# Performance work log

Measured on AMD Instinct MI355X. Metric: run time of the kernel, lower is better.

Reference implementation:

```python
import jax, jax.numpy as jnp
import numpy as np

BORDER = 3
SHIFTS = 2 * BORDER + 1  # 7 shifts per axis -> 49 total


def setup_inputs() -> dict:
    key = jax.random.key(0)
    k1, k2, k3 = jax.random.split(key, 3)
    B, C, H = 64, 1, 384
    sr = jax.random.normal(k1, (B, C, H, H), dtype=jnp.float32)
    hr = jax.random.normal(k2, (B, C, H, H), dtype=jnp.float32)
    hr_mask = (jax.random.uniform(k3, (B, C, H, H)) > 0.1).astype(jnp.float32)
    return {"sr": sr, "hr": hr, "hr_mask": hr_mask}


def _cmse_masked(sr, hr, hr_mask):
    B, C, H, _ = hr.shape
    crop = H - 2 * BORDER  # size_cropped_image
    # mask sr and hr as in the torch code (done once, outside the shift loop)
    sr_m = sr * hr_mask
    pred = sr_m[:, :, BORDER:H - BORDER, BORDER:H - BORDER]  # [B,C,crop,crop]
    hr_m = hr * hr_mask

    # all 49 (i,j) shift offsets
    ij = jnp.stack(
        jnp.meshgrid(jnp.arange(SHIFTS), jnp.arange(SHIFTS), indexing="ij"), axis=-1
    ).reshape(-1, 2)  # [49, 2]

    def per_shift(carry, off):
        i, j = off[0], off[1]
        L = jax.lax.dynamic_slice(hr_m, (0, 0, i, j), (B, C, crop, crop))
        m = jax.lax.dynamic_slice(hr_mask, (0, 0, i, j), (B, C, crop, crop))
        n = jnp.sum(m, axis=(1, 2, 3))  # total_pixels_masked per sample
        b = jnp.sum(L - pred, axis=(1, 2, 3)) / n  # brightness bias correction
        corrected = (pred + b[:, None, None, None]) * m
        mse = jnp.sum(jnp.square(L - corrected), axis=(1, 2, 3)) / n  # [B]
        return carry, mse

    _, mses = jax.lax.scan(per_shift, None, ij)  # [49, B]
    min_cmse = jnp.min(mses, axis=0)  # best shift per sample
    return jnp.mean(min_cmse)


def reference(sr, hr, hr_mask):
    return _cmse_masked(sr, hr, hr_mask)
```

## Files before the change

kernel.cpp:

```cpp
#include <hip/hip_runtime.h>

#define IMG   384
#define IMG4  96
#define IMG2  (IMG*IMG)
#define CROP  378
#define NB    64
#define NGRP  16
#define NROWS 24
#define NSTR  6
#define NTH   256
#define PSTR  520

typedef __fp16 half8  __attribute__((ext_vector_type(8)));
typedef __fp16 f16x2  __attribute__((ext_vector_type(2)));
typedef float  floatx4 __attribute__((ext_vector_type(4)));

__device__ __forceinline__ unsigned pkh(float a, float b) {
    f16x2 h = __builtin_amdgcn_cvt_pkrtz(a, b);
    return __builtin_bit_cast(unsigned, h);
}

__global__ __launch_bounds__(NTH)
void corr_kernel(const float* __restrict__ sr, const float* __restrict__ hr,
                 const float* __restrict__ mk, float* __restrict__ part)
{
    __shared__ __align__(16) char qpl [16*784];
    __shared__ __align__(16) char mpl [16*784];
    __shared__ __align__(16) char ppool[2*8*800 + 16];
    __shared__ float rowQ2[32];
    char* const ppl  = ppool;
    char* const p2pl = ppool + 8*800 + 16;

    const int tid = threadIdx.x;
    const int id  = blockIdx.x;
    const int c8  = id & 7;
    const int k0  = id >> 3;
    const int b   = c8 + 8 * (k0 >> 4);
    const int grp = k0 & 15;
    const int c0  = grp * NROWS;
    const int nvalid = (CROP - c0 < NROWS) ? (CROP - c0) : NROWS;

    const float*  sb   = sr + (size_t)b * IMG2;
    const float*  mown = mk + (size_t)b * IMG2;
    const float4* hb4  = (const float4*)(hr + (size_t)b * IMG2);
    const float4* mb4  = (const float4*)(mk + (size_t)b * IMG2);

    const int wid  = tid >> 6;
    const int lane = tid & 63;
    const int m16  = lane & 15;
    const int g    = lane >> 4;

    floatx4 D0 = {0.f, 0.f, 0.f, 0.f};
    floatx4 D1 = {0.f, 0.f, 0.f, 0.f};

    const uint4 onesbits = {0x3C003C00u, 0x3C003C00u, 0x3C003C00u, 0x3C003C00u};
    const uint4 zerobits = {0u, 0u, 0u, 0u};
    const half8 ones8 = __builtin_bit_cast(half8, onesbits);
    const half8 zero8 = __builtin_bit_cast(half8, zerobits);

    float eacc = 0.f;
    int ei = 0, et = 0, ek = 0, ecolByte = 0;
    if (tid < 252) {
        ei = tid / 36; const int rem = tid % 36; et = rem % 12; ek = rem / 12;
        const int ec = (et < 6) ? et : (372 + et);
        ecolByte = 2 * ec;
    }

    float4 hvr[2], mvr[2];
    auto qm_issue = [&](int relBase) {
        #pragma unroll
        for (int k = 0; k < 2; ++k) {
            const int idx = (tid + k * 256) % 384;
            const int rw = idx / 96, c = idx % 96;
            int w = c0 + relBase + rw; if (w > 383) w = 383;
            hvr[k] = hb4[(size_t)w * IMG4 + c];
            mvr[k] = mb4[(size_t)w * IMG4 + c];
        }
    };
    auto qm_write = [&](int relBase) {
        #pragma unroll
        for (int k = 0; k < 2; ++k) {
            const int idx = (tid + k * 256) % 384;
            const int rw = idx / 96, c = idx % 96;
            const int rel = relBase + rw;
            const float4 hv = hvr[k], mv = mvr[k];
            const float qx = hv.x*mv.x, qy = hv.y*mv.y;
            const float qz = hv.z*mv.z, qw = hv.w*mv.w;
            const int slot = rel & 15;
            *(uint2*)(qpl + slot*784 + c*8) = make_uint2(pkh(qx, qy), pkh(qz, qw));
            *(uint2*)(mpl + slot*784 + c*8) = make_uint2(pkh(mv.x, mv.y), pkh(mv.z, mv.w));
            if (k == 0 || tid < 128)
                atomicAdd(&rowQ2[rel & 31], qx*qx + qy*qy + qz*qz + qw*qw);
        }
    };
    float ps0[3], ps1[3], pm0[3], pm1[3];
    auto p_issue = [&](int relBase) {
        #pragma unroll
        for (int k = 0; k < 3; ++k) {
            const int idx = (tid + k * 256) % 756;
            const int rw = idx / 189, d = 4 + idx % 189;
            int rc = relBase + rw; if (c0 + rc > 377) rc = 377 - c0;
            const int v0 = 2*d - 8;
            const float* srow = sb   + (size_t)(c0 + rc + 3) * IMG + (v0 + 3);
            const float* mrow = mown + (size_t)(c0 + rc + 3) * IMG + (v0 + 3);
            ps0[k] = srow[0]; ps1[k] = srow[1];
            pm0[k] = mrow[0]; pm1[k] = mrow[1];
        }
    };
    auto p_write = [&](int relBase) {
        #pragma unroll
        for (int k = 0; k < 3; ++k) {
            const int idx = (tid + k * 256) % 756;
            const int rw = idx / 189, d = 4 + idx % 189;
            const int rrel = relBase + rw;
            const float p0 = ps0[k] * pm0[k], p1 = ps1[k] * pm1[k];
            const int slot = rrel & 7;
            *(unsigned*)(ppl  + slot*800 + 4*d) = pkh(p0, p1);
            *(unsigned*)(p2pl + slot*800 + 4*d) = pkh(p0*p0, p1*p1);
        }
    };

    for (int idx = tid; idx < 8*2*11; idx += NTH) {
        const int slot = idx / 22, rem = idx % 22;
        const int pl = rem / 11, kk = rem % 11;
        const int dd = (kk < 4) ? kk : (189 + kk);
        *(unsigned*)((pl ? p2pl : ppl) + slot*800 + 4*dd) = 0u;
    }
    if (tid < 32) rowQ2[tid] = 0.f;
    __syncthreads();
    for (int idx = tid; idx < 10*96; idx += NTH) {
        const int rw = idx / 96, c = idx % 96;
        int w = c0 + rw; if (w > 383) w = 383;
        const float4 hv = hb4[(size_t)w * IMG4 + c];
        const float4 mv = mb4[(size_t)w * IMG4 + c];
        const float qx = hv.x*mv.x, qy = hv.y*mv.y;
        const float qz = hv.z*mv.z, qw = hv.w*mv.w;
        *(uint2*)(qpl + rw*784 + c*8) = make_uint2(pkh(qx, qy), pkh(qz, qw));
        *(uint2*)(mpl + rw*784 + c*8) = make_uint2(pkh(mv.x, mv.y), pkh(mv.z, mv.w));
        atomicAdd(&rowQ2[rw], qx*qx + qy*qy + qz*qz + qw*qw);
    }
    p_issue(0);
    p_write(0);
    __syncthreads();

    for (int s = 0; s < NSTR; ++s) {
        const bool doStage = (s < NSTR - 1);
        if (doStage) {
            qm_issue(4*s + 10);
            p_issue(4*s + 4);
        }
        __builtin_amdgcn_sched_barrier(0);

        const int lr = 4*s + wid;
        if (lr < nvalid) {
            const int mm    = (m16 < 7) ? m16 : (m16 - 7);
            const int slotA = (lr + mm) & 15;
            const char* aB = ((m16 < 7) ? qpl : mpl) + slotA*784;
            const char* bB = ((m16 < 7) ? ppl : p2pl) + (lr & 7)*800;
            const int Sb = 16 - 2*mm + g*16;
            #pragma unroll
            for (int sl = 0; sl < 12; ++sl) {
                half8 av, bv;
                if (m16 < 14) {
                    av = *(const half8*)(aB + sl*64 + g*16);
                    const int S  = Sb + sl*64;
                    const int S0 = S & ~3;
                    const unsigned sh = (unsigned)((S & 2) << 3);
                    const unsigned* bw = (const unsigned*)(bB + S0);
                    const unsigned d0 = bw[0], d1 = bw[1], d2 = bw[2], d3 = bw[3], d4 = bw[4];
                    uint4 bi;
                    bi.x = __builtin_amdgcn_alignbit(d1, d0, sh);
                    bi.y = __builtin_amdgcn_alignbit(d2, d1, sh);
                    bi.z = __builtin_amdgcn_alignbit(d3, d2, sh);
                    bi.w = __builtin_amdgcn_alignbit(d4, d3, sh);
                    bv = __builtin_bit_cast(half8, bi);
                } else if (m16 == 14) {
                    av = ones8; bv = ones8;
                } else {
                    av = zero8; bv = zero8;
                }
                if (sl & 1) D1 = __builtin_amdgcn_mfma_f32_16x16x32_f16(av, bv, D1, 0, 0, 0);
                else        D0 = __builtin_amdgcn_mfma_f32_16x16x32_f16(av, bv, D0, 0, 0, 0);
            }
        }

        if (tid < 252) {
            #pragma unroll
            for (int rr = 0; rr < 4; ++rr) {
                if (4*s + rr < nvalid) {
                    const int slot = (4*s + rr + ei) & 15;
                    const char* pl = (ek == 0) ? mpl : qpl;
                    const float v = (float)*(const __fp16*)(pl + slot*784 + ecolByte);
                    eacc += (ek == 2) ? v*v : v;
                }
            }
        }

        if (doStage) {
            qm_write(4*s + 10);
            p_write(4*s + 4);
        }
        __syncthreads();
    }

    float* wred = (float*)ppool;
    {
        const floatx4 D = D0 + D1;
        const int rb = (lane >> 4) * 4, col = lane & 15;
        #pragma unroll
        for (int k = 0; k < 4; ++k)
            wred[wid*256 + (rb + k)*16 + col] = D[k];
    }
    __syncthreads();
    float* po = part + (size_t)(b * NGRP + grp) * PSTR;
    po[tid] = wred[tid] + wred[256 + tid] + wred[512 + tid] + wred[768 + tid];
    if (tid < 7) {
        float t = 0.f;
        for (int k = 0; k < nvalid; ++k) t += rowQ2[tid + k];
        po[256 + tid] = t;
    }
    if (tid < 252)
        po[264 + ek*84 + ei*12 + et] = eacc;
}

__global__ __launch_bounds__(NTH)
void mse_kernel(const float* __restrict__ part, double* __restrict__ bmin)
{
    __shared__ double chunk[4][49][7];
    const int b   = blockIdx.x;
    const int tid = threadIdx.x;
    const int s   = tid & 63;
    const int cc  = tid >> 6;

    if (s < 49) {
        const int i = s / 7, j = s % 7;
        double A=0, Bc=0, Cc=0, Tm=0, Tq=0, Tq2=0, Sp=0;
        for (int gg = cc*4; gg < cc*4 + 4; ++gg) {
            const float* p = part + (size_t)(b * NGRP + gg) * PSTR;
            A   += p[i*16 + j];
            Cc  += p[(7+i)*16 + j];
            Bc  += p[(7+i)*16 + 7 + j];
            Tq  += p[i*16 + 14];
            Tm  += p[(7+i)*16 + 14];
            Sp  += p[14*16 + 0];
            Tq2 += p[256 + i];
            #pragma unroll
            for (int t = 0; t < 12; ++t) {
                if (t < j || t >= j + 6) {
                    Tm  -= p[264 +      i*12 + t];
                    Tq  -= p[264 + 84 + i*12 + t];
                    Tq2 -= p[264 +168 + i*12 + t];
                }
            }
        }
        chunk[cc][s][0] = A;  chunk[cc][s][1] = Bc; chunk[cc][s][2] = Cc;
        chunk[cc][s][3] = Tm; chunk[cc][s][4] = Tq; chunk[cc][s][5] = Tq2;
        chunk[cc][s][6] = Sp;
    }
    __syncthreads();

    if (tid < 64) {
        double mse = 1e300;
        if (tid < 49) {
            double v[7];
            #pragma unroll
            for (int q = 0; q < 7; ++q)
                v[q] = chunk[0][tid][q] + chunk[1][tid][q] + chunk[2][tid][q] + chunk[3][tid][q];
            const double A = v[0], Bc = v[1], Cc = v[2], Tm = v[3];
            const double Tq = v[4], Tq2 = v[5], Sp = v[6];
            const double bb = (Tq - Sp) / Tm;
            mse = (Tq2 - 2.0*A - 2.0*bb*Tq + Bc + 2.0*bb*Cc + bb*bb*Tm) / Tm;
        }
        for (int off = 32; off; off >>= 1) {
            const double o = __shfl_down(mse, off);
            mse = fmin(mse, o);
        }
        if (tid == 0) bmin[b] = mse;
    }
}

__global__ __launch_bounds__(64)
void mean_kernel(const double* __restrict__ bmin, float* __restrict__ out)
{
    double v = bmin[threadIdx.x];
    for (int off = 32; off; off >>= 1) v += __shfl_down(v, off);
    if (threadIdx.x == 0) out[0] = (float)(v / 64.0);
}

extern "C" void kernel_launch(void* const* d_in, const int* in_sizes, int n_in,
                              void* d_out, int out_size, void* d_ws, size_t ws_size,
                              hipStream_t stream) {
    const float* sr = (const float*)d_in[0];
    const float* hr = (const float*)d_in[1];
    const float* mk = (const float*)d_in[2];

    float* part = (float*)d_ws;
    const size_t part_bytes = (size_t)NB * NGRP * PSTR * sizeof(float);
    double* bmin = (double*)((char*)d_ws + part_bytes);

    corr_kernel<<<dim3(NB * NGRP), NTH, 0, stream>>>(sr, hr, mk, part);
    mse_kernel<<<dim3(NB), NTH, 0, stream>>>(part, bmin);
    mean_kernel<<<dim3(1), 64, 0, stream>>>(bmin, (float*)d_out);
}
```

Baseline: 58.63 us.

## Replace pipelined row streaming with 512-thread three-tile load-then-compute loop

```diff
diff --git a/kernel.cpp b/kernel.cpp
--- a/kernel.cpp
+++ b/kernel.cpp
@@ -7,8 +7,9 @@
 #define NB    64
 #define NGRP  16
 #define NROWS 24
-#define NSTR  6
-#define NTH   256
+#define TILES 3
+#define TROWS 8
+#define NTH   512
 #define PSTR  520
 
 typedef __fp16 half8  __attribute__((ext_vector_type(8)));
@@ -24,10 +25,10 @@
 void corr_kernel(const float* __restrict__ sr, const float* __restrict__ hr,
                  const float* __restrict__ mk, float* __restrict__ part)
 {
-    __shared__ __align__(16) char qpl [16*784];
-    __shared__ __align__(16) char mpl [16*784];
+    __shared__ __align__(16) char qpl [15*784];
+    __shared__ __align__(16) char mpl [15*784];
     __shared__ __align__(16) char ppool[2*8*800 + 16];
-    __shared__ float rowQ2[32];
+    __shared__ float rowQ2[TILES][16];
     char* const ppl  = ppool;
     char* const p2pl = ppool + 8*800 + 16;
 
@@ -66,97 +67,45 @@
         ecolByte = 2 * ec;
     }
 
-    float4 hvr[2], mvr[2];
-    auto qm_issue = [&](int relBase) {
-        #pragma unroll
-        for (int k = 0; k < 2; ++k) {
-            const int idx = (tid + k * 256) % 384;
+    if (tid < TILES*16) ((float*)rowQ2)[tid] = 0.f;
+    if (tid < 8*2*11) {
+        const int slot = tid / 22, rem = tid % 22;
+        const int pl = rem / 11, kk = rem % 11;
+        const int dd = (kk < 4) ? kk : (189 + kk);
+        *(unsigned*)((pl ? p2pl : ppl) + slot*800 + 4*dd) = 0u;
+    }
+    __syncthreads();
+
+    for (int t = 0; t < TILES; ++t) {
+        const int r0 = TROWS * t;
+
+        for (int idx = tid; idx < 15*96; idx += NTH) {
             const int rw = idx / 96, c = idx % 96;
-            int w = c0 + relBase + rw; if (w > 383) w = 383;
-            hvr[k] = hb4[(size_t)w * IMG4 + c];
-            mvr[k] = mb4[(size_t)w * IMG4 + c];
-        }
-    };
-    auto qm_write = [&](int relBase) {
-        #pragma unroll
-        for (int k = 0; k < 2; ++k) {
-            const int idx = (tid + k * 256) % 384;
-            const int rw = idx / 96, c = idx % 96;
-            const int rel = relBase + rw;
-            const float4 hv = hvr[k], mv = mvr[k];
+            int w = c0 + r0 + rw; if (w > 383) w = 383;
+            const float4 hv = hb4[(size_t)w * IMG4 + c];
+            const float4 mv = mb4[(size_t)w * IMG4 + c];
             const float qx = hv.x*mv.x, qy = hv.y*mv.y;
             const float qz = hv.z*mv.z, qw = hv.w*mv.w;
-            const int slot = rel & 15;
-            *(uint2*)(qpl + slot*784 + c*8) = make_uint2(pkh(qx, qy), pkh(qz, qw));
-            *(uint2*)(mpl + slot*784 + c*8) = make_uint2(pkh(mv.x, mv.y), pkh(mv.z, mv.w));
-            if (k == 0 || tid < 128)
-                atomicAdd(&rowQ2[rel & 31], qx*qx + qy*qy + qz*qz + qw*qw);
-        }
-    };
-    float ps0[3], ps1[3], pm0[3], pm1[3];
-    auto p_issue = [&](int relBase) {
-        #pragma unroll
-        for (int k = 0; k < 3; ++k) {
-            const int idx = (tid + k * 256) % 756;
+            *(uint2*)(qpl + rw*784 + c*8) = make_uint2(pkh(qx, qy), pkh(qz, qw));
+            *(uint2*)(mpl + rw*784 + c*8) = make_uint2(pkh(mv.x, mv.y), pkh(mv.z, mv.w));
+            atomicAdd(&rowQ2[t][rw], qx*qx + qy*qy + qz*qz + qw*qw);
+        }
+        for (int idx = tid; idx < 8*189; idx += NTH) {
             const int rw = idx / 189, d = 4 + idx % 189;
-            int rc = relBase + rw; if (c0 + rc > 377) rc = 377 - c0;
+            int rc = r0 + rw; if (c0 + rc > 377) rc = 377 - c0;
             const int v0 = 2*d - 8;
             const float* srow = sb   + (size_t)(c0 + rc + 3) * IMG + (v0 + 3);
             const float* mrow = mown + (size_t)(c0 + rc + 3) * IMG + (v0 + 3);
-            ps0[k] = srow[0]; ps1[k] = srow[1];
-            pm0[k] = mrow[0]; pm1[k] = mrow[1];
-        }
-    };
-    auto p_write = [&](int relBase) {
-        #pragma unroll
-        for (int k = 0; k < 3; ++k) {
-            const int idx = (tid + k * 256) % 756;
-            const int rw = idx / 189, d = 4 + idx % 189;
-            const int rrel = relBase + rw;
-            const float p0 = ps0[k] * pm0[k], p1 = ps1[k] * pm1[k];
-            const int slot = rrel & 7;
-            *(unsigned*)(ppl  + slot*800 + 4*d) = pkh(p0, p1);
-            *(unsigned*)(p2pl + slot*800 + 4*d) = pkh(p0*p0, p1*p1);
-        }
-    };
-
-    for (int idx = tid; idx < 8*2*11; idx += NTH) {
-        const int slot = idx / 22, rem = idx % 22;
-        const int pl = rem / 11, kk = rem % 11;
-        const int dd = (kk < 4) ? kk : (189 + kk);
-        *(unsigned*)((pl ? p2pl : ppl) + slot*800 + 4*dd) = 0u;
-    }
-    if (tid < 32) rowQ2[tid] = 0.f;
-    __syncthreads();
-    for (int idx = tid; idx < 10*96; idx += NTH) {
-        const int rw = idx / 96, c = idx % 96;
-        int w = c0 + rw; if (w > 383) w = 383;
-        const float4 hv = hb4[(size_t)w * IMG4 + c];
-        const float4 mv = mb4[(size_t)w * IMG4 + c];
-        const float qx = hv.x*mv.x, qy = hv.y*mv.y;
-        const float qz = hv.z*mv.z, qw = hv.w*mv.w;
-        *(uint2*)(qpl + rw*784 + c*8) = make_uint2(pkh(qx, qy), pkh(qz, qw));
-        *(uint2*)(mpl + rw*784 + c*8) = make_uint2(pkh(mv.x, mv.y), pkh(mv.z, mv.w));
-        atomicAdd(&rowQ2[rw], qx*qx + qy*qy + qz*qz + qw*qw);
-    }
-    p_issue(0);
-    p_write(0);
-    __syncthreads();
-
-    for (int s = 0; s < NSTR; ++s) {
-        const bool doStage = (s < NSTR - 1);
-        if (doStage) {
-            qm_issue(4*s + 10);
-            p_issue(4*s + 4);
-        }
-        __builtin_amdgcn_sched_barrier(0);
-
-        const int lr = 4*s + wid;
-        if (lr < nvalid) {
-            const int mm    = (m16 < 7) ? m16 : (m16 - 7);
-            const int slotA = (lr + mm) & 15;
-            const char* aB = ((m16 < 7) ? qpl : mpl) + slotA*784;
-            const char* bB = ((m16 < 7) ? ppl : p2pl) + (lr & 7)*800;
+            const float p0 = srow[0] * mrow[0], p1 = srow[1] * mrow[1];
+            *(unsigned*)(ppl  + rw*800 + 4*d) = pkh(p0, p1);
+            *(unsigned*)(p2pl + rw*800 + 4*d) = pkh(p0*p0, p1*p1);
+        }
+        __syncthreads();
+
+        if (r0 + wid < nvalid) {
+            const int mm = (m16 < 7) ? m16 : (m16 - 7);
+            const char* aB = ((m16 < 7) ? qpl : mpl) + (wid + mm)*784;
+            const char* bB = ((m16 < 7) ? ppl : p2pl) + wid*800;
             const int Sb = 16 - 2*mm + g*16;
             #pragma unroll
             for (int sl = 0; sl < 12; ++sl) {
@@ -186,19 +135,14 @@
 
         if (tid < 252) {
             #pragma unroll
-            for (int rr = 0; rr < 4; ++rr) {
-                if (4*s + rr < nvalid) {
-                    const int slot = (4*s + rr + ei) & 15;
+            for (int rr = 0; rr < TROWS; ++rr) {
+                if (r0 + rr < nvalid) {
+                    const int slot = rr + ei;
                     const char* pl = (ek == 0) ? mpl : qpl;
                     const float v = (float)*(const __fp16*)(pl + slot*784 + ecolByte);
                     eacc += (ek == 2) ? v*v : v;
                 }
             }
-        }
-
-        if (doStage) {
-            qm_write(4*s + 10);
-            p_write(4*s + 4);
         }
         __syncthreads();
     }
@@ -213,17 +157,26 @@
     }
     __syncthreads();
     float* po = part + (size_t)(b * NGRP + grp) * PSTR;
-    po[tid] = wred[tid] + wred[256 + tid] + wred[512 + tid] + wred[768 + tid];
+    if (tid < 256) {
+        float v = 0.f;
+        #pragma unroll
+        for (int w = 0; w < 8; ++w) v += wred[w*256 + tid];
+        po[tid] = v;
+    }
     if (tid < 7) {
-        float t = 0.f;
-        for (int k = 0; k < nvalid; ++k) t += rowQ2[tid + k];
-        po[256 + tid] = t;
+        float acc = 0.f;
+        for (int t = 0; t < TILES; ++t) {
+            int vt = nvalid - TROWS*t;
+            vt = (vt < 0) ? 0 : (vt > TROWS ? TROWS : vt);
+            for (int k = 0; k < vt; ++k) acc += rowQ2[t][tid + k];
+        }
+        po[256 + tid] = acc;
     }
     if (tid < 252)
         po[264 + ek*84 + ei*12 + et] = eacc;
 }
 
-__global__ __launch_bounds__(NTH)
+__global__ __launch_bounds__(256)
 void mse_kernel(const float* __restrict__ part, double* __restrict__ bmin)
 {
     __shared__ double chunk[4][49][7];
@@ -299,6 +252,6 @@
     double* bmin = (double*)((char*)d_ws + part_bytes);
 
     corr_kernel<<<dim3(NB * NGRP), NTH, 0, stream>>>(sr, hr, mk, part);
-    mse_kernel<<<dim3(NB), NTH, 0, stream>>>(part, bmin);
+    mse_kernel<<<dim3(NB), 256, 0, stream>>>(part, bmin);
     mean_kernel<<<dim3(1), 64, 0, stream>>>(bmin, (float*)d_out);
 }
```

Result: slower. 70.33 us (+20.0%).
